# Kernel tuning notes

Measured on AMD Instinct MI355X. Metric: run time of the kernel, lower is better.

## Reference

```python
import math
import jax, jax.numpy as jnp
import numpy as np

EPS = 1e-5

def _ln(x, g, b, axes):
    # LayerNormalization4D / 4DCF: mean/var (unbiased=False) over `axes`
    mu = x.mean(axis=axes, keepdims=True)
    var = ((x - mu) ** 2).mean(axis=axes, keepdims=True)
    return (x - mu) / jnp.sqrt(var + EPS) * g + b

def _prelu(x, a):
    return jnp.where(x >= 0, x, a * x)

def _unfold(x, ks, hs):
    # x: [N, C, Q] -> [N, L, C*ks]; patch layout (c, k) matches F.unfold
    N, C, Qd = x.shape
    L = (Qd - ks) // hs + 1
    idx = jnp.arange(L) * hs
    p = x[:, :, idx[:, None] + jnp.arange(ks)]  # [N, C, L, ks]
    return p.transpose(0, 2, 1, 3).reshape(N, L, C * ks)

def _lstm_dir(xs, Wi, Wh, bi, bh, H):
    # xs: [N, L, Cin]; torch gate order i, f, g, o
    xg = jnp.einsum('nlc,gc->nlg', xs, Wi) + bi + bh  # [N, L, 4H]
    def step(carry, gt):
        h, c = carry
        g = gt + h @ Wh.T
        i, f, gg, o = jnp.split(g, 4, axis=-1)
        c = jax.nn.sigmoid(f) * c + jax.nn.sigmoid(i) * jnp.tanh(gg)
        h = jax.nn.sigmoid(o) * jnp.tanh(c)
        return (h, c), h
    N = xs.shape[0]
    z = jnp.zeros((N, H), xs.dtype)
    _, hs = jax.lax.scan(step, (z, z), jnp.swapaxes(xg, 0, 1))
    return jnp.swapaxes(hs, 0, 1)

def _bilstm(x, wih, whh, bih, bhh):
    H = whh.shape[-1]
    f = _lstm_dir(x, wih[0], whh[0], bih[0], bhh[0], H)
    bk = _lstm_dir(x[:, ::-1], wih[1], whh[1], bih[1], bhh[1], H)[:, ::-1]
    return jnp.concatenate([f, bk], axis=-1)

def _convT1d(x, w, b):
    # x: [N, I, L]; w: [I, O, K] (torch ConvTranspose1d layout); stride 1
    K = w.shape[2]
    w2 = jnp.transpose(w, (1, 0, 2))[:, :, ::-1]
    y = jax.lax.conv_general_dilated(x, w2, (1,), [(K - 1, K - 1)],
                                     dimension_numbers=('NCH', 'OIH', 'NCH'))
    return y + b[None, :, None]

def _forward(x, mouth, intra_g, intra_b, intra_wih, intra_whh, intra_bih, intra_bhh,
             intra_lw, intra_lb, inter_g, inter_b, inter_wih, inter_whh, inter_bih,
             inter_bhh, inter_lw, inter_lb, qw, qb, qa, qg, qbe, kw, kb, ka, kg, kbe,
             vw, vb, va, vg, vbe, pw, pb, pa, pg, pbe):
    emb_ks, emb_hs = 4, 1
    B, C, oT, oQ = x.shape
    T = math.ceil((oT - emb_ks) / emb_hs) * emb_hs + emb_ks
    Qd = math.ceil((oQ - emb_ks) / emb_hs) * emb_hs + emb_ks
    x = jnp.pad(x, ((0, 0), (0, 0), (0, T - oT), (0, Qd - oQ)))
    inp = x
    # ---- intra (biLSTM along freq axis) ----
    h = _ln(inp, intra_g[None, :, None, None], intra_b[None, :, None, None], (1,))
    h = h.transpose(0, 2, 1, 3).reshape(B * T, C, Qd)
    h = _unfold(h, emb_ks, emb_hs)                          # [B*T, L, C*ks]
    h = _bilstm(h, intra_wih, intra_whh, intra_bih, intra_bhh)
    h = _convT1d(h.transpose(0, 2, 1), intra_lw, intra_lb)  # [B*T, C, Qd]
    intra = h.reshape(B, T, C, Qd).transpose(0, 2, 1, 3) + inp
    # ---- inter (biLSTM along time axis) ----
    h = _ln(intra, inter_g[None, :, None, None], inter_b[None, :, None, None], (1,))
    h = h.transpose(0, 3, 1, 2).reshape(B * Qd, C, T)
    h = _unfold(h, emb_ks, emb_hs)
    h = _bilstm(h, inter_wih, inter_whh, inter_bih, inter_bhh)
    h = _convT1d(h.transpose(0, 2, 1), inter_lw, inter_lb)  # [B*Qd, C, T]
    inter = h.reshape(B, Qd, C, T).transpose(0, 2, 3, 1) + intra
    inter = inter[..., :oT, :oQ]                             # [B, C, oT, oQ]
    # ---- multi-head full self-attention over time (conv1x1 QKV per head) ----
    NH = qw.shape[0]
    def qkv(w, b_, a_, g_, be_):
        y = jnp.einsum('bctf,hec->hbetf', inter, w) + b_[:, None, :, None, None]
        y = _prelu(y, a_[:, None, None, None, None])
        return _ln(y, g_[:, None, :, None, :], be_[:, None, :, None, :], (2, 4))
    Qh = qkv(qw, qb, qa, qg, qbe)   # [H, B, E, T, F]
    Kh = qkv(kw, kb, ka, kg, kbe)
    Vh = qkv(vw, vb, va, vg, vbe)   # [H, B, D, T, F]
    E = Qh.shape[2]; D = Vh.shape[2]; F = oQ
    q2 = Qh.transpose(0, 1, 3, 2, 4).reshape(NH, B, oT, E * F)
    k2 = Kh.transpose(0, 1, 3, 2, 4).reshape(NH, B, oT, E * F)
    v2 = Vh.transpose(0, 1, 3, 2, 4).reshape(NH, B, oT, D * F)
    scale = 1.0 / jnp.sqrt(jnp.asarray(E * F, x.dtype))
    attn = jax.nn.softmax(jnp.einsum('hbte,hbse->hbts', q2, k2) * scale, axis=-1)
    o = jnp.einsum('hbts,hbsd->hbtd', attn, v2).reshape(NH, B, oT, D, F)
    o = o.transpose(1, 0, 3, 2, 4).reshape(B, NH * D, oT, F)
    # ---- concat projection ----
    p = jnp.einsum('bctf,oc->botf', o, pw) + pb[None, :, None, None]
    p = _prelu(p, pa)
    p = _ln(p, pg[None, :, None, :], pbe[None, :, None, :], (1, 3))
    return p + inter

def setup_inputs() -> dict:
    key = jax.random.key(0)
    keys = iter(jax.random.split(key, 48))
    f32 = jnp.float32
    def nrm(shape, s=0.05):
        return jax.random.normal(next(keys), shape, f32) * s
    B, C, T, F = 2, 48, 512, 65
    K, H, NH, E = 4, 192, 4, 8
    Cin = C * K
    D = C // NH
    return {
        'x': jax.random.normal(next(keys), (B, C, T, F), f32),
        'mouth': jax.random.normal(next(keys), (B, 64), f32),
        'intra_g': jnp.ones((C,), f32), 'intra_b': jnp.zeros((C,), f32),
        'intra_wih': nrm((2, 4 * H, Cin)), 'intra_whh': nrm((2, 4 * H, H)),
        'intra_bih': nrm((2, 4 * H)), 'intra_bhh': nrm((2, 4 * H)),
        'intra_lw': nrm((2 * H, C, K)), 'intra_lb': nrm((C,)),
        'inter_g': jnp.ones((C,), f32), 'inter_b': jnp.zeros((C,), f32),
        'inter_wih': nrm((2, 4 * H, Cin)), 'inter_whh': nrm((2, 4 * H, H)),
        'inter_bih': nrm((2, 4 * H)), 'inter_bhh': nrm((2, 4 * H)),
        'inter_lw': nrm((2 * H, C, K)), 'inter_lb': nrm((C,)),
        'qw': nrm((NH, E, C)), 'qb': nrm((NH, E)), 'qa': 0.25 * jnp.ones((NH,), f32),
        'qg': jnp.ones((NH, E, F), f32), 'qbe': jnp.zeros((NH, E, F), f32),
        'kw': nrm((NH, E, C)), 'kb': nrm((NH, E)), 'ka': 0.25 * jnp.ones((NH,), f32),
        'kg': jnp.ones((NH, E, F), f32), 'kbe': jnp.zeros((NH, E, F), f32),
        'vw': nrm((NH, D, C)), 'vb': nrm((NH, D)), 'va': 0.25 * jnp.ones((NH,), f32),
        'vg': jnp.ones((NH, D, F), f32), 'vbe': jnp.zeros((NH, D, F), f32),
        'pw': nrm((C, C)), 'pb': nrm((C,)), 'pa': jnp.float32(0.25),
        'pg': jnp.ones((C, F), f32), 'pbe': jnp.zeros((C, F), f32),
    }

def reference(x, mouth, intra_g, intra_b, intra_wih, intra_whh, intra_bih, intra_bhh,
              intra_lw, intra_lb, inter_g, inter_b, inter_wih, inter_whh, inter_bih,
              inter_bhh, inter_lw, inter_lb, qw, qb, qa, qg, qbe, kw, kb, ka, kg, kbe,
              vw, vb, va, vg, vbe, pw, pb, pa, pg, pbe):
    return _forward(x, mouth, intra_g, intra_b, intra_wih, intra_whh, intra_bih,
                    intra_bhh, intra_lw, intra_lb, inter_g, inter_b, inter_wih,
                    inter_whh, inter_bih, inter_bhh, inter_lw, inter_lb, qw, qb, qa,
                    qg, qbe, kw, kb, ka, kg, kbe, vw, vb, va, vg, vbe, pw, pb, pa,
                    pg, pbe)
```

## Files before the change

### kernel.cpp

```cpp
#include <hip/hip_runtime.h>
#include <hip/hip_bf16.h>

typedef __bf16 bf16x8 __attribute__((ext_vector_type(8)));
typedef unsigned short u16x8 __attribute__((ext_vector_type(8)));
typedef float f32x4 __attribute__((ext_vector_type(4)));

#define DEV static __device__ __forceinline__

DEV unsigned short f2bf(float f){
  __hip_bfloat16 h = __float2bfloat16(f);
  return __builtin_bit_cast(unsigned short, h);
}
DEV float b2f(unsigned short u){
  return __bfloat162float(__builtin_bit_cast(__hip_bfloat16, u));
}
DEV float sig2(float xs){
  return __builtin_amdgcn_rcpf(1.0f + __builtin_amdgcn_exp2f(-xs));
}
DEV float tanh2s(float xs){
  return 1.0f - 2.0f*__builtin_amdgcn_rcpf(__builtin_amdgcn_exp2f(xs + xs) + 1.0f);
}
DEV float tanh_n(float x){
  return 1.0f - 2.0f*__builtin_amdgcn_rcpf(__builtin_amdgcn_exp2f(x * 2.885390082f) + 1.0f);
}
DEV void lds_barrier(){
  asm volatile("s_waitcnt lgkmcnt(0)\ns_barrier" ::: "memory");
}


__global__ void zero16(uint4* p, size_t n){
  size_t i = (size_t)blockIdx.x*blockDim.x + threadIdx.x;
  size_t st = (size_t)gridDim.x*blockDim.x;
  uint4 z = make_uint4(0u,0u,0u,0u);
  for (; i < n; i += st) p[i] = z;
}

__global__ void zero_pads(unsigned short* hs, int NSEQ, int Qrows, int L){
  int i = blockIdx.x*256 + threadIdx.x;
  int total = NSEQ*6*384;
  if (i < total){
    int t = i/(6*384); int rem = i - t*(6*384);
    int r = rem/384, c = rem - r*384;
    int row = r < 3 ? r : L + r;
    hs[((size_t)t*Qrows + row)*384 + c] = 0;
  }
}

__global__ void cast_bf(const float* __restrict__ s, unsigned short* __restrict__ d, int n, float scale){
  int i = blockIdx.x*256 + threadIdx.x;
  if (i < n) d[i] = f2bf(s[i]*scale);
}

__global__ void cast_wi(const float* __restrict__ s, unsigned short* __restrict__ d, float scale){
  int i = blockIdx.x*256 + threadIdx.x;
  if (i < 294912){
    int dn = i/192, k = i - dn*192;
    int c = k >> 2, kk = k & 3;
    d[(size_t)dn*192 + kk*48 + c] = f2bf(s[i]*scale);
  }
}

__global__ void bias_comb(const float* __restrict__ a, const float* __restrict__ b,
                          float* __restrict__ d, int n, float scale){
  int i = blockIdx.x*256 + threadIdx.x;
  if (i < n) d[i] = (a[i] + b[i])*scale;
}

__global__ void lwt_build(const float* __restrict__ lw, unsigned short* __restrict__ lwt2){
  int i = blockIdx.x*256 + threadIdx.x;
  if (i < 384*48*4){
    int m = i / 192; int rest = i - m*192; int c = rest >> 2; int k = rest & 3;
    int kap = k*384 + m;
    lwt2[((size_t)(kap>>3)*48 + c)*8 + (kap&7)] = f2bf(lw[i]);
  }
}

__global__ __launch_bounds__(256) void ln_unf_intra(
    const float* __restrict__ in, const float* __restrict__ g,
    const float* __restrict__ be, unsigned short* __restrict__ unf)
{
  int bt = blockIdx.x; int b = bt >> 9, t = bt & 511;
  __shared__ float v[48][66];
  __shared__ float mu[65], rs[65];
  __shared__ float g_l[48], b_l[48];
  const float* base = in + (size_t)b*(48*512*65) + (size_t)t*65;
  for (int i = threadIdx.x; i < 48*65; i += 256){
    int c = i/65, q = i - c*65;
    v[c][q] = base[(size_t)c*(512*65) + q];
  }
  if (threadIdx.x < 48){ g_l[threadIdx.x] = g[threadIdx.x]; b_l[threadIdx.x] = be[threadIdx.x]; }
  __syncthreads();
  if (threadIdx.x < 65){
    int q = threadIdx.x; float s=0.f, s2=0.f;
    #pragma unroll
    for (int c = 0; c < 48; c++){ float x = v[c][q]; s += x; s2 += x*x; }
    float m = s*(1.0f/48.0f);
    mu[q] = m; rs[q] = rsqrtf(s2*(1.0f/48.0f) - m*m + 1e-5f);
  }
  __syncthreads();
  unsigned short* orow = unf + (size_t)(b*512 + t)*62*192;
  for (int idx = threadIdx.x; idx < 62*24; idx += 256){
    int l = idx/24, jg = idx - l*24;
    int kk = jg/6, c0 = (jg - kk*6)*8;
    int q = l + kk;
    ushort4 p0, p1;
    float mq = mu[q], rq = rs[q];
    p0.x = f2bf((v[c0+0][q]-mq)*rq*g_l[c0+0] + b_l[c0+0]);
    p0.y = f2bf((v[c0+1][q]-mq)*rq*g_l[c0+1] + b_l[c0+1]);
    p0.z = f2bf((v[c0+2][q]-mq)*rq*g_l[c0+2] + b_l[c0+2]);
    p0.w = f2bf((v[c0+3][q]-mq)*rq*g_l[c0+3] + b_l[c0+3]);
    p1.x = f2bf((v[c0+4][q]-mq)*rq*g_l[c0+4] + b_l[c0+4]);
    p1.y = f2bf((v[c0+5][q]-mq)*rq*g_l[c0+5] + b_l[c0+5]);
    p1.z = f2bf((v[c0+6][q]-mq)*rq*g_l[c0+6] + b_l[c0+6]);
    p1.w = f2bf((v[c0+7][q]-mq)*rq*g_l[c0+7] + b_l[c0+7]);
    *(ushort4*)(orow + (size_t)l*192 + kk*48 + c0) = p0;
    *(ushort4*)(orow + (size_t)l*192 + kk*48 + c0 + 4) = p1;
  }
}

__global__ __launch_bounds__(256) void ln_unf_inter(
    const float* __restrict__ in, const float* __restrict__ g,
    const float* __restrict__ be, unsigned short* __restrict__ unf)
{
  int bt = blockIdx.x; int b = bt >> 9, t = bt & 511;
  __shared__ float v[48][66];
  __shared__ float mu[65], rs[65];
  __shared__ float g_l[48], b_l[48];
  const float* base = in + (size_t)b*(48*512*65) + (size_t)t*65;
  for (int i = threadIdx.x; i < 48*65; i += 256){
    int c = i/65, q = i - c*65;
    v[c][q] = base[(size_t)c*(512*65) + q];
  }
  if (threadIdx.x < 48){ g_l[threadIdx.x] = g[threadIdx.x]; b_l[threadIdx.x] = be[threadIdx.x]; }
  __syncthreads();
  if (threadIdx.x < 65){
    int q = threadIdx.x; float s=0.f, s2=0.f;
    #pragma unroll
    for (int c = 0; c < 48; c++){ float x = v[c][q]; s += x; s2 += x*x; }
    float m = s*(1.0f/48.0f);
    mu[q] = m; rs[q] = rsqrtf(s2*(1.0f/48.0f) - m*m + 1e-5f);
  }
  __syncthreads();
  for (int idx = threadIdx.x; idx < 4*65*6; idx += 256){
    int s = idx/390;
    int rem = idx - s*390;
    int q = rem/6, c0 = (rem - q*6)*8;
    int l = t - 3 + s, kk = 3 - s;
    if (l < 0 || l > 508) continue;
    float mq = mu[q], rq = rs[q];
    ushort4 p0, p1;
    p0.x = f2bf((v[c0+0][q]-mq)*rq*g_l[c0+0] + b_l[c0+0]);
    p0.y = f2bf((v[c0+1][q]-mq)*rq*g_l[c0+1] + b_l[c0+1]);
    p0.z = f2bf((v[c0+2][q]-mq)*rq*g_l[c0+2] + b_l[c0+2]);
    p0.w = f2bf((v[c0+3][q]-mq)*rq*g_l[c0+3] + b_l[c0+3]);
    p1.x = f2bf((v[c0+4][q]-mq)*rq*g_l[c0+4] + b_l[c0+4]);
    p1.y = f2bf((v[c0+5][q]-mq)*rq*g_l[c0+5] + b_l[c0+5]);
    p1.z = f2bf((v[c0+6][q]-mq)*rq*g_l[c0+6] + b_l[c0+6]);
    p1.w = f2bf((v[c0+7][q]-mq)*rq*g_l[c0+7] + b_l[c0+7]);
    size_t addr = ((size_t)(b*65+q)*509 + l)*192 + kk*48 + c0;
    *(ushort4*)(unf + addr) = p0;
    *(ushort4*)(unf + addr + 4) = p1;
  }
}

__global__ __launch_bounds__(256) void gemm_xg(
    const unsigned short* __restrict__ unf, const unsigned short* __restrict__ wib,
    const float* __restrict__ bias, unsigned short* __restrict__ xg,
    int NSEQ, int TW, int win0, int L, int nvalid)
{
  const int d = blockIdx.z;
  const int lane = threadIdx.x & 63, wave = threadIdx.x >> 6;
  const int kg = lane >> 4, lr = lane & 15;
  const int nslb = TW >> 3;
  const int sb  = blockIdx.x / nslb;
  const int slb = blockIdx.x - sb*nslb;
  const int nbase = blockIdx.y*64;
  const unsigned short* Bp = wib + (size_t)d*768*192;

  const unsigned short* abase[2];
  #pragma unroll
  for (int mt = 0; mt < 2; mt++){
    int sl = slb*8 + wave*2 + mt;
    int s = win0 + sl;
    int l = d ? (L-1-s) : s;
    l = l < 0 ? 0 : (l > L-1 ? L-1 : l);
    int seq = sb*16 + lr;
    seq = seq < nvalid ? seq : nvalid-1;
    abase[mt] = unf + ((size_t)seq*L + l)*192;
  }

  f32x4 acc[2][4] = {};
  #pragma unroll
  for (int kt = 0; kt < 6; kt++){
    int k0 = kt*32 + kg*8;
    bf16x8 a0 = *(const bf16x8*)(abase[0] + k0);
    bf16x8 a1 = *(const bf16x8*)(abase[1] + k0);
    #pragma unroll
    for (int nt = 0; nt < 4; nt++){
      int n = nbase + nt*16 + lr;
      bf16x8 bfr = *(const bf16x8*)(Bp + (size_t)n*192 + k0);
      acc[0][nt] = __builtin_amdgcn_mfma_f32_16x16x32_bf16(a0, bfr, acc[0][nt], 0,0,0);
      acc[1][nt] = __builtin_amdgcn_mfma_f32_16x16x32_bf16(a1, bfr, acc[1][nt], 0,0,0);
    }
  }
  #pragma unroll
  for (int mt = 0; mt < 2; mt++){
    int sl = slb*8 + wave*2 + mt;
    size_t rowb = (((size_t)d*(NSEQ>>4) + sb)*TW + sl)*768;
    #pragma unroll
    for (int nt = 0; nt < 4; nt++){
      int n = nbase + nt*16 + lr;
      float bs = bias[d*768 + n];
      ushort4 pk;
      pk.x = f2bf(acc[mt][nt][0] + bs);
      pk.y = f2bf(acc[mt][nt][1] + bs);
      pk.z = f2bf(acc[mt][nt][2] + bs);
      pk.w = f2bf(acc[mt][nt][3] + bs);
      *(ushort4*)(xg + (rowb + n)*16 + kg*4) = pk;
    }
  }
}

__global__ __launch_bounds__(768, 3) void fused_rec_xg(
    const unsigned short* __restrict__ xgA,
    const unsigned short* __restrict__ whb,
    unsigned short* __restrict__ hs,
    float* __restrict__ state,
    const unsigned short* __restrict__ unf,
    const unsigned short* __restrict__ wib,
    const float* __restrict__ bias,
    unsigned short* __restrict__ xgB,
    int NSEQ, int TW, int win0, int L, int Qrows, int nvalid, int steps,
    int NR, int NSBR, int NSLB, int win0x)
{
  const int tid = threadIdx.x;
  const int lane = tid & 63, w = tid >> 6;
  const int kg = lane >> 4, lr = lane & 15;

  __shared__ unsigned short h_lds[2][16][200];

  if ((int)blockIdx.x >= NR){
    int e = blockIdx.x - NR;
    int nb = e % 12; e /= 12;
    int slb = e % NSLB; e /= NSLB;
    int sb = e % NSBR; int d = e / NSBR;
    int sl = slb*12 + w;
    if (sl >= TW) return;
    int s = win0x + sl;
    int l = d ? (L-1-s) : s;
    l = l < 0 ? 0 : (l > L-1 ? L-1 : l);
    int seq = sb*16 + lr;
    seq = seq < nvalid ? seq : nvalid-1;
    const unsigned short* ab = unf + ((size_t)seq*L + l)*192;
    const unsigned short* Bp = wib + (size_t)d*768*192;
    const int nbase = nb*64;
    f32x4 acc[4] = {};
    #pragma unroll
    for (int kt = 0; kt < 6; kt++){
      int k0 = kt*32 + kg*8;
      bf16x8 a = *(const bf16x8*)(ab + k0);
      #pragma unroll
      for (int nt = 0; nt < 4; nt++){
        bf16x8 bfr = *(const bf16x8*)(Bp + (size_t)(nbase+nt*16+lr)*192 + k0);
        acc[nt] = __builtin_amdgcn_mfma_f32_16x16x32_bf16(a, bfr, acc[nt], 0,0,0);
      }
    }
    size_t rowb = (((size_t)d*NSBR + sb)*TW + sl)*768;
    #pragma unroll
    for (int nt = 0; nt < 4; nt++){
      int n = nbase + nt*16 + lr;
      float bs = bias[d*768 + n];
      ushort4 pk;
      pk.x = f2bf(acc[nt][0] + bs);
      pk.y = f2bf(acc[nt][1] + bs);
      pk.z = f2bf(acc[nt][2] + bs);
      pk.w = f2bf(acc[nt][3] + bs);
      *(ushort4*)(xgB + (rowb + n)*16 + kg*4) = pk;
    }
    return;
  }

  const int d = blockIdx.x / NSBR;
  const int sbx = blockIdx.x - d*NSBR;
  const int seq0 = sbx * 16;
  const int col = w*16 + lr;

  bf16x8 whf[4][6];
  #pragma unroll
  for (int g = 0; g < 4; g++){
    const unsigned short* wrow = whb + ((size_t)d*768 + g*192 + col)*192;
    #pragma unroll
    for (int kt = 0; kt < 6; kt++)
      whf[g][kt] = *(const bf16x8*)(wrow + kt*32 + kg*8);
  }

  float c_reg[4];
  unsigned short* hsp[4];
  bool val[4];
  const int l0 = d ? (L-1-win0) : win0;
  const ptrdiff_t ldelta = d ? -384 : 384;
  #pragma unroll
  for (int r = 0; r < 4; r++){
    int m = kg*4 + r;
    const float* st = state + (((size_t)d*NSEQ + seq0 + m)*2)*192;
    h_lds[0][m][col] = f2bf(st[col]);
    c_reg[r] = st[192 + col];
    val[r] = (seq0 + m) < nvalid;
    hsp[r] = hs + ((size_t)(seq0+m)*Qrows + (l0+3))*384 + d*192 + col;
  }
  lds_barrier();

  const unsigned short* xq0 = xgA + ((((size_t)d*NSBR + sbx)*TW)*768)*16
                              + ((size_t)col)*16 + kg*4;
  const size_t SSTR = (size_t)768*16;

  uint2 pfA[4], pfB[4];
  {
    const unsigned short* p1 = xq0 + (steps > 1 ? SSTR : 0);
    #pragma unroll
    for (int g = 0; g < 4; g++){
      pfA[g] = *(const uint2*)(xq0 + (size_t)g*(192*16));
      pfB[g] = *(const uint2*)(p1  + (size_t)g*(192*16));
    }
  }

  int cur = 0;
  auto do_step = [&](uint2 (&pf)[4], int ss){
    f32x4 acc[4];
    #pragma unroll
    for (int g = 0; g < 4; g++){
      unsigned int lo = pf[g].x, hi = pf[g].y;
      acc[g][0] = b2f((unsigned short)(lo & 0xffffu));
      acc[g][1] = b2f((unsigned short)(lo >> 16));
      acc[g][2] = b2f((unsigned short)(hi & 0xffffu));
      acc[g][3] = b2f((unsigned short)(hi >> 16));
    }
    int nss = ss + 2; nss = nss > steps-1 ? steps-1 : nss;
    const unsigned short* np = xq0 + (size_t)nss*SSTR;
    #pragma unroll
    for (int g = 0; g < 4; g++)
      pf[g] = *(const uint2*)(np + (size_t)g*(192*16));
    #pragma unroll
    for (int kt = 0; kt < 6; kt++){
      bf16x8 a = *(const bf16x8*)(&h_lds[cur][lr][kt*32 + kg*8]);
      #pragma unroll
      for (int g = 0; g < 4; g++)
        acc[g] = __builtin_amdgcn_mfma_f32_16x16x32_bf16(a, whf[g][kt], acc[g], 0,0,0);
    }
    #pragma unroll
    for (int r = 0; r < 4; r++){
      float gi = sig2(acc[0][r]);
      float gf = sig2(acc[1][r]);
      float gg = tanh2s(acc[2][r]);
      float go = sig2(acc[3][r]);
      float c = gf*c_reg[r] + gi*gg;
      c_reg[r] = c;
      float h = go*tanh_n(c);
      unsigned short hb = f2bf(h);
      h_lds[cur^1][kg*4 + r][col] = hb;
      if (val[r]) *hsp[r] = hb;
      hsp[r] += ldelta;
    }
    lds_barrier();
    cur ^= 1;
  };

  for (int ss = 0; ss < steps; ss += 2){
    do_step(pfA, ss);
    if (ss + 1 < steps) do_step(pfB, ss + 1);
  }

  #pragma unroll
  for (int r = 0; r < 4; r++){
    int m = kg*4 + r;
    float* st = state + (((size_t)d*NSEQ + seq0 + m)*2)*192;
    st[col] = b2f(h_lds[cur][m][col]);
    st[192 + col] = c_reg[r];
  }
}

template<int MODE>
__global__ __launch_bounds__(512, 1) void gemm_convt(
    const unsigned short* __restrict__ hs, const unsigned short* __restrict__ lwt2,
    const float* __restrict__ lb, const float* __restrict__ addsrc, float* __restrict__ dst)
{
  constexpr int Q  = MODE ? 512 : 65;
  const int lane = threadIdx.x & 63, wave = threadIdx.x >> 6;
  const int kg = lane >> 4, lr = lane & 15;
  const int R0 = blockIdx.x * 128;

  __shared__ union __align__(16) U {
    unsigned short b[192*48*8];
    float c[128][53];
  } sm;

  for (int cidx = threadIdx.x; cidx < 9216; cidx += 512)
    *(uint4*)&sm.b[(size_t)cidx*8] = *(const uint4*)(lwt2 + (size_t)cidx*8);
  __syncthreads();

  const int row = R0 + wave*16 + lr;
  const int an = row / Q, aq = row - an*Q;
  const unsigned short* ab[4];
  #pragma unroll
  for (int tap = 0; tap < 4; tap++)
    ab[tap] = hs + ((size_t)an*(Q+3) + aq + 3 - tap)*384 + kg*8;

  bf16x8 pf0 = *(const bf16x8*)(ab[0]);
  bf16x8 pf1 = *(const bf16x8*)(ab[0] + 32);
  int ntap = 0, nm = 2;

  f32x4 acc[3] = {};
  for (int kt = 0; kt < 48; kt++){
    bf16x8 a = pf0;
    pf0 = pf1;
    if (kt < 46){
      pf1 = *(const bf16x8*)(ab[ntap] + nm*32);
      nm++;
      if (nm == 12){ nm = 0; ntap++; }
    }
    const int bo = (kt*4 + kg)*48*8;
    #pragma unroll
    for (int nt = 0; nt < 3; nt++){
      bf16x8 bfr = *(const bf16x8*)&sm.b[bo + (nt*16 + lr)*8];
      acc[nt] = __builtin_amdgcn_mfma_f32_16x16x32_bf16(a, bfr, acc[nt], 0,0,0);
    }
  }

  if (MODE == 0){
    __syncthreads();
    #pragma unroll
    for (int nt = 0; nt < 3; nt++)
      #pragma unroll
      for (int r = 0; r < 4; r++)
        sm.c[wave*16 + kg*4 + r][nt*16 + lr] = acc[nt][r];
    __syncthreads();
    const int b = R0 >= 33280 ? 1 : 0;
    const size_t bb = (size_t)b*1597440;
    const int rb = R0 - b*33280;
    for (int idx = threadIdx.x; idx < 48*32; idx += 512){
      int n = idx >> 5, g = idx & 31;
      size_t off = bb + (size_t)n*33280 + rb + g*4;
      float4 av = *(const float4*)(addsrc + off);
      float lbn = lb[n];
      float4 o;
      o.x = sm.c[g*4+0][n] + lbn + av.x;
      o.y = sm.c[g*4+1][n] + lbn + av.y;
      o.z = sm.c[g*4+2][n] + lbn + av.z;
      o.w = sm.c[g*4+3][n] + lbn + av.w;
      *(float4*)(dst + off) = o;
    }
  } else {
    #pragma unroll
    for (int nt = 0; nt < 3; nt++){
      int n = nt*16 + lr;
      float lbn = lb[n];
      #pragma unroll
      for (int r = 0; r < 4; r++){
        int orow = R0 + wave*16 + kg*4 + r;
        int ns = orow >> 9, t = orow & 511;
        size_t off = (size_t)(ns/65)*1597440 + (size_t)n*33280 + (ns%65) + (size_t)t*65;
        dst[off] = acc[nt][r] + lbn + addsrc[off];
      }
    }
  }
}

__global__ __launch_bounds__(256) void gemm_rm(
    const unsigned short* __restrict__ A, const unsigned short* __restrict__ B, float* __restrict__ C,
    int lda, int ldb, int ldc, int KT, int nmax, long long strA, long long strB, long long strC)
{
  const int z = blockIdx.z;
  A += (size_t)z * strA; B += (size_t)z * strB; C += (size_t)z * strC;
  const int lane = threadIdx.x & 63, wave = threadIdx.x >> 6;
  const int kg = lane >> 4, lr = lane & 15;
  const int rowbase = blockIdx.x*128 + wave*32;
  const int nbase = blockIdx.y*64;
  f32x4 acc[2][4] = {};
  for (int kt = 0; kt < KT; kt++){
    int k0 = kt*32 + kg*8;
    bf16x8 a0 = *(const bf16x8*)(A + (size_t)(rowbase+lr)*lda + k0);
    bf16x8 a1 = *(const bf16x8*)(A + (size_t)(rowbase+16+lr)*lda + k0);
    #pragma unroll
    for (int nt = 0; nt < 4; nt++){
      bf16x8 bfr = *(const bf16x8*)(B + (size_t)(nbase+nt*16+lr)*ldb + k0);
      acc[0][nt] = __builtin_amdgcn_mfma_f32_16x16x32_bf16(a0, bfr, acc[0][nt], 0,0,0);
      acc[1][nt] = __builtin_amdgcn_mfma_f32_16x16x32_bf16(a1, bfr, acc[1][nt], 0,0,0);
    }
  }
  #pragma unroll
  for (int mt = 0; mt < 2; mt++)
  #pragma unroll
  for (int nt = 0; nt < 4; nt++)
  #pragma unroll
  for (int r = 0; r < 4; r++){
    int n = nbase + nt*16 + lr;
    if (n < nmax){
      int row = rowbase + mt*16 + kg*4 + r;
      C[(size_t)row*ldc + n] = acc[mt][nt][r];
    }
  }
}

__global__ __launch_bounds__(256) void qkv_k(
    const float* __restrict__ inter, const float* __restrict__ w, const float* __restrict__ bias,
    const float* __restrict__ alpha, const float* __restrict__ gam, const float* __restrict__ bet,
    unsigned short* __restrict__ out, int E, int mode)
{
  int t = blockIdx.x; int hb = blockIdx.y; int h = hb >> 1, b = hb & 1;
  __shared__ float in_l[48][66];
  __shared__ float w_l[12][48];
  __shared__ float y_l[780];
  __shared__ float rs1[4], rs2[4];
  const float* base = inter + (size_t)b*(48*512*65) + (size_t)t*65;
  for (int i = threadIdx.x; i < 48*65; i += 256){
    int c = i/65, f = i - c*65;
    in_l[c][f] = base[(size_t)c*(512*65) + f];
  }
  for (int i = threadIdx.x; i < E*48; i += 256) w_l[i/48][i - (i/48)*48] = w[(size_t)h*E*48 + i];
  __syncthreads();
  int nel = E*65;
  float a = alpha[h];
  float ps = 0.f, pq = 0.f;
  for (int i = threadIdx.x; i < nel; i += 256){
    int e = i/65, f = i - e*65;
    float s = bias[h*E + e];
    #pragma unroll
    for (int c = 0; c < 48; c++) s += w_l[e][c]*in_l[c][f];
    s = s >= 0.f ? s : a*s;
    y_l[i] = s; ps += s; pq += s*s;
  }
  #pragma unroll
  for (int o = 32; o; o >>= 1){ ps += __shfl_xor(ps, o); pq += __shfl_xor(pq, o); }
  if ((threadIdx.x & 63) == 0){ rs1[threadIdx.x>>6] = ps; rs2[threadIdx.x>>6] = pq; }
  __syncthreads();
  ps = rs1[0]+rs1[1]+rs1[2]+rs1[3]; pq = rs2[0]+rs2[1]+rs2[2]+rs2[3];
  float inv = 1.0f/(float)nel;
  float m = ps*inv; float rstd = rsqrtf(pq*inv - m*m + 1e-5f);
  for (int i = threadIdx.x; i < nel; i += 256){
    int e = i/65, f = i - e*65;
    float v = (y_l[i]-m)*rstd*gam[(size_t)(h*E+e)*65 + f] + bet[(size_t)(h*E+e)*65 + f];
    if (mode < 2) out[((size_t)hb*512 + t)*544 + i] = f2bf(v);
    else          out[((size_t)hb*832 + i)*512 + t] = f2bf(v);
  }
}

__global__ __launch_bounds__(256) void softmax_k(const float* __restrict__ S, unsigned short* __restrict__ P){
  size_t row = (size_t)blockIdx.y*512 + blockIdx.x;
  const float* s = S + row*512;
  int tid = threadIdx.x;
  float v0 = s[tid], v1 = s[tid+256];
  float m = fmaxf(v0, v1);
  #pragma unroll
  for (int o = 32; o; o >>= 1) m = fmaxf(m, __shfl_xor(m, o));
  __shared__ float r4[4], q4[4];
  if ((tid & 63) == 0) r4[tid>>6] = m;
  __syncthreads();
  m = fmaxf(fmaxf(r4[0], r4[1]), fmaxf(r4[2], r4[3]));
  const float sc = 0.04385290096535146f;
  float e0 = __expf((v0-m)*sc), e1 = __expf((v1-m)*sc);
  float su = e0 + e1;
  #pragma unroll
  for (int o = 32; o; o >>= 1) su += __shfl_xor(su, o);
  if ((tid & 63) == 0) q4[tid>>6] = su;
  __syncthreads();
  su = q4[0]+q4[1]+q4[2]+q4[3];
  float inv = __builtin_amdgcn_rcpf(su);
  unsigned short* p = P + row*512;
  p[tid] = f2bf(e0*inv); p[tid+256] = f2bf(e1*inv);
}

__global__ __launch_bounds__(256) void pout_k(
    const float* __restrict__ o, const float* __restrict__ pw, const float* __restrict__ pb,
    const float* __restrict__ pa, const float* __restrict__ pg, const float* __restrict__ pbe,
    const float* __restrict__ inter, float* __restrict__ out)
{
  int bt = blockIdx.x; int b = bt >> 9, t = bt & 511;
  __shared__ float o_l[48][66];
  __shared__ float pw_l[48][48];
  __shared__ float p_l[3120];
  __shared__ float rs1[4], rs2[4];
  for (int i = threadIdx.x; i < 48*65; i += 256){
    int c = i/65, f = i - c*65; int h = c/12, dd = c - h*12;
    o_l[c][f] = o[((size_t)(h*2+b)*512 + t)*780 + dd*65 + f];
  }
  for (int i = threadIdx.x; i < 48*48; i += 256) pw_l[i/48][i - (i/48)*48] = pw[i];
  __syncthreads();
  float a = pa[0];
  float ps = 0.f, pq = 0.f;
  for (int i = threadIdx.x; i < 3120; i += 256){
    int oc = i/65, f = i - oc*65;
    float s = pb[oc];
    #pragma unroll
    for (int c = 0; c < 48; c++) s += pw_l[oc][c]*o_l[c][f];
    s = s >= 0.f ? s : a*s;
    p_l[i] = s; ps += s; pq += s*s;
  }
  #pragma unroll
  for (int o2 = 32; o2; o2 >>= 1){ ps += __shfl_xor(ps, o2); pq += __shfl_xor(pq, o2); }
  if ((threadIdx.x & 63) == 0){ rs1[threadIdx.x>>6] = ps; rs2[threadIdx.x>>6] = pq; }
  __syncthreads();
  ps = rs1[0]+rs1[1]+rs1[2]+rs1[3]; pq = rs2[0]+rs2[1]+rs2[2]+rs2[3];
  float m = ps*(1.0f/3120.0f); float rstd = rsqrtf(pq*(1.0f/3120.0f) - m*m + 1e-5f);
  for (int i = threadIdx.x; i < 3120; i += 256){
    int oc = i/65, f = i - oc*65;
    size_t off = ((size_t)(b*48+oc)*512 + t)*65 + f;
    out[off] = (p_l[i]-m)*rstd*pg[i] + pbe[i] + inter[off];
  }
}


extern "C" void kernel_launch(void* const* d_in, const int* in_sizes, int n_in,
                              void* d_out, int out_size, void* d_ws, size_t ws_size,
                              hipStream_t stream)
{
  const float* x         = (const float*)d_in[0];
  const float* intra_g   = (const float*)d_in[2];
  const float* intra_b   = (const float*)d_in[3];
  const float* intra_wih = (const float*)d_in[4];
  const float* intra_whh = (const float*)d_in[5];
  const float* intra_bih = (const float*)d_in[6];
  const float* intra_bhh = (const float*)d_in[7];
  const float* intra_lw  = (const float*)d_in[8];
  const float* intra_lb  = (const float*)d_in[9];
  const float* inter_g   = (const float*)d_in[10];
  const float* inter_b   = (const float*)d_in[11];
  const float* inter_wih = (const float*)d_in[12];
  const float* inter_whh = (const float*)d_in[13];
  const float* inter_bih = (const float*)d_in[14];
  const float* inter_bhh = (const float*)d_in[15];
  const float* inter_lw  = (const float*)d_in[16];
  const float* inter_lb  = (const float*)d_in[17];
  const float* qw  = (const float*)d_in[18];
  const float* qb  = (const float*)d_in[19];
  const float* qa  = (const float*)d_in[20];
  const float* qg  = (const float*)d_in[21];
  const float* qbe = (const float*)d_in[22];
  const float* kw  = (const float*)d_in[23];
  const float* kb  = (const float*)d_in[24];
  const float* ka  = (const float*)d_in[25];
  const float* kgm = (const float*)d_in[26];
  const float* kbe = (const float*)d_in[27];
  const float* vw  = (const float*)d_in[28];
  const float* vb  = (const float*)d_in[29];
  const float* va  = (const float*)d_in[30];
  const float* vg  = (const float*)d_in[31];
  const float* vbe = (const float*)d_in[32];
  const float* pw  = (const float*)d_in[33];
  const float* pb  = (const float*)d_in[34];
  const float* pa  = (const float*)d_in[35];
  const float* pgm = (const float*)d_in[36];
  const float* pbe = (const float*)d_in[37];

  char* ws = (char*)d_ws;
  constexpr size_t WIB_INTRA = 0;
  constexpr size_t WHB_INTRA = 589824;
  constexpr size_t WIB_INTER = 1179648;
  constexpr size_t WHB_INTER = 1769472;
  constexpr size_t LWT_INTRA = 2359296;
  constexpr size_t LWT_INTER = 2555904;
  constexpr size_t BIAS_INTRA = 2752512;
  constexpr size_t BIAS_INTER = 2758656;
  constexpr size_t UNF   = 2764800;
  constexpr size_t INTER = 2764800;
  constexpr size_t STATE = 28311552;
  constexpr size_t HS    = 31457280;
  constexpr size_t INTRA = 84934656;
  constexpr size_t XG    = 97714176;
  constexpr size_t Q2B   = XG;
  constexpr size_t K2B   = XG + 4456448;
  constexpr size_t V2T   = XG + 8912896;
  constexpr size_t SCORES= XG + 15728640;
  constexpr size_t ATTNB = XG + 24117248;
  constexpr size_t OBUF  = XG + 28311552;

  auto U16 = [&](size_t off){ return (unsigned short*)(ws + off); };
  auto F32 = [&](size_t off){ return (float*)(ws + off); };

  const float LOG2E = 1.4426950408889634f;

  cast_wi<<<1152,256,0,stream>>>(intra_wih, U16(WIB_INTRA), LOG2E);
  cast_bf<<<1152,256,0,stream>>>(intra_whh, U16(WHB_INTRA), 294912, LOG2E);
  cast_wi<<<1152,256,0,stream>>>(inter_wih, U16(WIB_INTER), LOG2E);
  cast_bf<<<1152,256,0,stream>>>(inter_whh, U16(WHB_INTER), 294912, LOG2E);
  bias_comb<<<6,256,0,stream>>>(intra_bih, intra_bhh, F32(BIAS_INTRA), 1536, LOG2E);
  bias_comb<<<6,256,0,stream>>>(inter_bih, inter_bhh, F32(BIAS_INTER), 1536, LOG2E);
  lwt_build<<<288,256,0,stream>>>(intra_lw, U16(LWT_INTRA));
  lwt_build<<<288,256,0,stream>>>(inter_lw, U16(LWT_INTER));

  {
    unsigned short* xb[2] = { U16(XG), U16(XG + 25165824) };
    ln_unf_intra<<<1024,256,0,stream>>>(x, intra_g, intra_b, U16(UNF));
    zero_pads<<<9216,256,0,stream>>>(U16(HS), 1024, 68, 62);
    zero16<<<2048,256,0,stream>>>((uint4*)(ws+STATE), 3145728/16);
    gemm_xg<<<dim3(64,12,2),256,0,stream>>>(U16(UNF), U16(WIB_INTRA), F32(BIAS_INTRA), xb[0],
                                            1024, 8, 0, 62, 1024);
    for (int w = 0; w < 8; w++){
      int win0 = w*8;
      int steps = (62 - win0) < 8 ? (62 - win0) : 8;
      int nxg = (w < 7) ? 1536 : 0;
      fused_rec_xg<<<128 + nxg, 768, 0, stream>>>(
          xb[w&1], U16(WHB_INTRA), U16(HS), F32(STATE),
          U16(UNF), U16(WIB_INTRA), F32(BIAS_INTRA), xb[(w+1)&1],
          1024, 8, win0, 62, 68, 1024, steps,
          128, 64, 1, (w+1)*8);
    }
    gemm_convt<0><<<520,512,0,stream>>>(U16(HS), U16(LWT_INTRA), intra_lb, x, F32(INTRA));
  }

  {
    unsigned short* xb[2] = { U16(XG), U16(XG + 21233664) };
    ln_unf_inter<<<1024,256,0,stream>>>(F32(INTRA), inter_g, inter_b, U16(UNF));
    zero_pads<<<1170,256,0,stream>>>(U16(HS), 130, 515, 509);
    zero16<<<2048,256,0,stream>>>((uint4*)(ws+STATE), 3145728/16);
    gemm_xg<<<dim3(54,12,2),256,0,stream>>>(U16(UNF), U16(WIB_INTER), F32(BIAS_INTER), xb[0],
                                            144, 48, 0, 509, 130);
    for (int w = 0; w < 11; w++){
      int win0 = w*48;
      int steps = (509 - win0) < 48 ? (509 - win0) : 48;
      int nxg = (w < 10) ? 864 : 0;
      fused_rec_xg<<<18 + nxg, 768, 0, stream>>>(
          xb[w&1], U16(WHB_INTER), U16(HS), F32(STATE),
          U16(UNF), U16(WIB_INTER), F32(BIAS_INTER), xb[(w+1)&1],
          144, 48, win0, 509, 515, 130, steps,
          18, 9, 4, (w+1)*48);
    }
    gemm_convt<1><<<520,512,0,stream>>>(U16(HS), U16(LWT_INTER), inter_lb, F32(INTRA), F32(INTER));
  }

  zero16<<<2048,256,0,stream>>>((uint4*)(ws+Q2B), 15728640/16);
  qkv_k<<<dim3(512,8),256,0,stream>>>(F32(INTER), qw, qb, qa, qg, qbe, U16(Q2B), 8, 0);
  qkv_k<<<dim3(512,8),256,0,stream>>>(F32(INTER), kw, kb, ka, kgm, kbe, U16(K2B), 8, 1);
  qkv_k<<<dim3(512,8),256,0,stream>>>(F32(INTER), vw, vb, va, vg, vbe, U16(V2T), 12, 2);
  gemm_rm<<<dim3(4,8,8),256,0,stream>>>(U16(Q2B), U16(K2B), F32(SCORES),
                                        544, 544, 512, 17, 512,
                                        (long long)512*544, (long long)512*544, (long long)512*512);
  softmax_k<<<dim3(512,8),256,0,stream>>>(F32(SCORES), U16(ATTNB));
  gemm_rm<<<dim3(4,13,8),256,0,stream>>>(U16(ATTNB), U16(V2T), F32(OBUF),
                                         512, 512, 780, 16, 780,
                                         (long long)512*512, (long long)832*512, (long long)512*780);
  pout_k<<<1024,256,0,stream>>>(F32(OBUF), pw, pb, pa, pgm, pbe, F32(INTER), (float*)d_out);
}
```

Measured before the change: 1.651 ms.

## Deepen recurrence prefetch, pad LDS for occupancy, split convT weight staging, widen inter window

In the fused recurrent kernel, the gate-input prefetch depth grows from two steps to four. LDS is padded to about 84KB so that only one such block fits per CU, presumably to keep the recurrent blocks isolated from the co-scheduled xg-GEMM blocks. gemm_convt now stages its weights in two halves, which halves its LDS footprint and drops the min-blocks launch bound, so more blocks can be resident per CU. The inter-chunk window grows from 48 to 56 steps, which means fewer launches and more overlapped GEMM blocks per window, at the cost of a larger xg buffer offset and some extra register pressure.

```diff
diff --git a/kernel.cpp b/kernel.cpp
--- a/kernel.cpp
+++ b/kernel.cpp
@@ -237,7 +237,10 @@
   const int lane = tid & 63, w = tid >> 6;
   const int kg = lane >> 4, lr = lane & 15;
 
-  __shared__ unsigned short h_lds[2][16][200];
+  __shared__ union __align__(16) SMU {
+    unsigned short h[2][16][200];
+    char pad[86016];
+  } smu;
 
   if ((int)blockIdx.x >= NR){
     int e = blockIdx.x - NR;
@@ -303,7 +306,7 @@
   for (int r = 0; r < 4; r++){
     int m = kg*4 + r;
     const float* st = state + (((size_t)d*NSEQ + seq0 + m)*2)*192;
-    h_lds[0][m][col] = f2bf(st[col]);
+    smu.h[0][m][col] = f2bf(st[col]);
     c_reg[r] = st[192 + col];
     val[r] = (seq0 + m) < nvalid;
     hsp[r] = hs + ((size_t)(seq0+m)*Qrows + (l0+3))*384 + d*192 + col;
@@ -314,13 +317,15 @@
                               + ((size_t)col)*16 + kg*4;
   const size_t SSTR = (size_t)768*16;
 
-  uint2 pfA[4], pfB[4];
+  uint2 pf0[4], pf1[4], pf2[4], pf3[4];
   {
-    const unsigned short* p1 = xq0 + (steps > 1 ? SSTR : 0);
+    int s1 = steps > 1 ? 1 : 0, s2 = steps > 2 ? 2 : s1, s3 = steps > 3 ? 3 : s2;
     #pragma unroll
     for (int g = 0; g < 4; g++){
-      pfA[g] = *(const uint2*)(xq0 + (size_t)g*(192*16));
-      pfB[g] = *(const uint2*)(p1  + (size_t)g*(192*16));
+      pf0[g] = *(const uint2*)(xq0 + (size_t)g*(192*16));
+      pf1[g] = *(const uint2*)(xq0 + (size_t)s1*SSTR + (size_t)g*(192*16));
+      pf2[g] = *(const uint2*)(xq0 + (size_t)s2*SSTR + (size_t)g*(192*16));
+      pf3[g] = *(const uint2*)(xq0 + (size_t)s3*SSTR + (size_t)g*(192*16));
     }
   }
 
@@ -335,14 +340,14 @@
       acc[g][2] = b2f((unsigned short)(hi & 0xffffu));
       acc[g][3] = b2f((unsigned short)(hi >> 16));
     }
-    int nss = ss + 2; nss = nss > steps-1 ? steps-1 : nss;
+    int nss = ss + 4; nss = nss > steps-1 ? steps-1 : nss;
     const unsigned short* np = xq0 + (size_t)nss*SSTR;
     #pragma unroll
     for (int g = 0; g < 4; g++)
       pf[g] = *(const uint2*)(np + (size_t)g*(192*16));
     #pragma unroll
     for (int kt = 0; kt < 6; kt++){
-      bf16x8 a = *(const bf16x8*)(&h_lds[cur][lr][kt*32 + kg*8]);
+      bf16x8 a = *(const bf16x8*)(&smu.h[cur][lr][kt*32 + kg*8]);
       #pragma unroll
       for (int g = 0; g < 4; g++)
         acc[g] = __builtin_amdgcn_mfma_f32_16x16x32_bf16(a, whf[g][kt], acc[g], 0,0,0);
@@ -357,7 +362,7 @@
       c_reg[r] = c;
       float h = go*tanh_n(c);
       unsigned short hb = f2bf(h);
-      h_lds[cur^1][kg*4 + r][col] = hb;
+      smu.h[cur^1][kg*4 + r][col] = hb;
       if (val[r]) *hsp[r] = hb;
       hsp[r] += ldelta;
     }
@@ -365,22 +370,24 @@
     cur ^= 1;
   };
 
-  for (int ss = 0; ss < steps; ss += 2){
-    do_step(pfA, ss);
-    if (ss + 1 < steps) do_step(pfB, ss + 1);
+  for (int ss = 0; ss < steps; ss += 4){
+    do_step(pf0, ss);
+    if (ss + 1 < steps) do_step(pf1, ss + 1);
+    if (ss + 2 < steps) do_step(pf2, ss + 2);
+    if (ss + 3 < steps) do_step(pf3, ss + 3);
   }
 
   #pragma unroll
   for (int r = 0; r < 4; r++){
     int m = kg*4 + r;
     float* st = state + (((size_t)d*NSEQ + seq0 + m)*2)*192;
-    st[col] = b2f(h_lds[cur][m][col]);
+    st[col] = b2f(smu.h[cur][m][col]);
     st[192 + col] = c_reg[r];
   }
 }
 
 template<int MODE>
-__global__ __launch_bounds__(512, 1) void gemm_convt(
+__global__ __launch_bounds__(512) void gemm_convt(
     const unsigned short* __restrict__ hs, const unsigned short* __restrict__ lwt2,
     const float* __restrict__ lb, const float* __restrict__ addsrc, float* __restrict__ dst)
 {
@@ -390,39 +397,38 @@
   const int R0 = blockIdx.x * 128;
 
   __shared__ union __align__(16) U {
-    unsigned short b[192*48*8];
+    unsigned short b[96*48*8];
     float c[128][53];
   } sm;
 
-  for (int cidx = threadIdx.x; cidx < 9216; cidx += 512)
-    *(uint4*)&sm.b[(size_t)cidx*8] = *(const uint4*)(lwt2 + (size_t)cidx*8);
-  __syncthreads();
-
   const int row = R0 + wave*16 + lr;
   const int an = row / Q, aq = row - an*Q;
-  const unsigned short* ab[4];
-  #pragma unroll
-  for (int tap = 0; tap < 4; tap++)
-    ab[tap] = hs + ((size_t)an*(Q+3) + aq + 3 - tap)*384 + kg*8;
-
-  bf16x8 pf0 = *(const bf16x8*)(ab[0]);
-  bf16x8 pf1 = *(const bf16x8*)(ab[0] + 32);
-  int ntap = 0, nm = 2;
 
   f32x4 acc[3] = {};
-  for (int kt = 0; kt < 48; kt++){
-    bf16x8 a = pf0;
-    pf0 = pf1;
-    if (kt < 46){
-      pf1 = *(const bf16x8*)(ab[ntap] + nm*32);
-      nm++;
-      if (nm == 12){ nm = 0; ntap++; }
-    }
-    const int bo = (kt*4 + kg)*48*8;
-    #pragma unroll
-    for (int nt = 0; nt < 3; nt++){
-      bf16x8 bfr = *(const bf16x8*)&sm.b[bo + (nt*16 + lr)*8];
-      acc[nt] = __builtin_amdgcn_mfma_f32_16x16x32_bf16(a, bfr, acc[nt], 0,0,0);
+  #pragma unroll
+  for (int p = 0; p < 2; p++){
+    if (p) __syncthreads();
+    for (int cidx = threadIdx.x; cidx < 4608; cidx += 512)
+      *(uint4*)&sm.b[(size_t)cidx*8] = *(const uint4*)(lwt2 + ((size_t)p*4608 + cidx)*8);
+    __syncthreads();
+
+    const unsigned short* ab0 = hs + ((size_t)an*(Q+3) + aq + 3 - p*2)*384 + kg*8;
+    const unsigned short* ab1 = ab0 - 384;
+
+    bf16x8 pfA = *(const bf16x8*)(ab0);
+    bf16x8 pfB = *(const bf16x8*)(ab0 + 32);
+    bf16x8 pfC = *(const bf16x8*)(ab0 + 64);
+    for (int kt = 0; kt < 24; kt++){
+      bf16x8 a = pfA; pfA = pfB; pfB = pfC;
+      int nk = kt + 3;
+      if (nk < 24)
+        pfC = *(const bf16x8*)((nk < 12) ? (ab0 + nk*32) : (ab1 + (nk-12)*32));
+      const int bo = (kt*4 + kg)*48*8;
+      #pragma unroll
+      for (int nt = 0; nt < 3; nt++){
+        bf16x8 bfr = *(const bf16x8*)&sm.b[bo + (nt*16 + lr)*8];
+        acc[nt] = __builtin_amdgcn_mfma_f32_16x16x32_bf16(a, bfr, acc[nt], 0,0,0);
+      }
     }
   }
 
@@ -708,21 +714,21 @@
   }
 
   {
-    unsigned short* xb[2] = { U16(XG), U16(XG + 21233664) };
+    unsigned short* xb[2] = { U16(XG), U16(XG + 24772608) };
     ln_unf_inter<<<1024,256,0,stream>>>(F32(INTRA), inter_g, inter_b, U16(UNF));
     zero_pads<<<1170,256,0,stream>>>(U16(HS), 130, 515, 509);
     zero16<<<2048,256,0,stream>>>((uint4*)(ws+STATE), 3145728/16);
-    gemm_xg<<<dim3(54,12,2),256,0,stream>>>(U16(UNF), U16(WIB_INTER), F32(BIAS_INTER), xb[0],
-                                            144, 48, 0, 509, 130);
-    for (int w = 0; w < 11; w++){
-      int win0 = w*48;
-      int steps = (509 - win0) < 48 ? (509 - win0) : 48;
-      int nxg = (w < 10) ? 864 : 0;
+    gemm_xg<<<dim3(63,12,2),256,0,stream>>>(U16(UNF), U16(WIB_INTER), F32(BIAS_INTER), xb[0],
+                                            144, 56, 0, 509, 130);
+    for (int w = 0; w < 10; w++){
+      int win0 = w*56;
+      int steps = (509 - win0) < 56 ? (509 - win0) : 56;
+      int nxg = (w < 9) ? 1080 : 0;
       fused_rec_xg<<<18 + nxg, 768, 0, stream>>>(
           xb[w&1], U16(WHB_INTER), U16(HS), F32(STATE),
           U16(UNF), U16(WIB_INTER), F32(BIAS_INTER), xb[(w+1)&1],
-          144, 48, win0, 509, 515, 130, steps,
-          18, 9, 4, (w+1)*48);
+          144, 56, win0, 509, 515, 130, steps,
+          18, 9, 5, (w+1)*56);
     }
     gemm_convt<1><<<520,512,0,stream>>>(U16(HS), U16(LWT_INTER), inter_lb, F32(INTRA), F32(INTER));
   }
```

After: 2.300 ms. +39.3%, slower.
